# Optimization experiments

Hardware: AMD Instinct MI355X
Metric: run time of the kernel (lower is better)

Reference implementation:

```python
import jax, jax.numpy as jnp
import numpy as np

N_AGENTS = 64
_adj = np.ones((N_AGENTS, N_AGENTS)) - np.eye(N_AGENTS)
SEND_NP, RECV_NP = np.where(_adj)  # 4032 directed edges, no self-loops
N_EDGES = SEND_NP.shape[0]

D_NODE = 16
H = 64
D_OUT = 16
N_TYPES = 2
BATCH = 128


def _glorot(key, shape):
    fan_in, fan_out = shape[0], shape[1]
    lim = np.sqrt(6.0 / (fan_in + fan_out)).astype(np.float32)
    return jax.random.uniform(key, shape, jnp.float32, -lim, lim)


def setup_inputs() -> dict:
    key = jax.random.key(0)
    ks = jax.random.split(key, 16)
    inp = {
        "node_states": jax.random.normal(ks[0], (BATCH, N_AGENTS, 1, D_NODE), jnp.float32),
        "edge_types": jax.random.uniform(ks[1], (BATCH, N_EDGES, N_TYPES + 1, 1), jnp.float32),
        # edge encoder 0: MLP(32 -> 64 -> 64)
        "e0_w1": _glorot(ks[2], (2 * D_NODE, H)), "e0_b1": jnp.zeros((H,), jnp.float32),
        "e0_w2": _glorot(ks[3], (H, H)), "e0_b2": jnp.zeros((H,), jnp.float32),
        # edge encoder 1
        "e1_w1": _glorot(ks[4], (2 * D_NODE, H)), "e1_b1": jnp.zeros((H,), jnp.float32),
        "e1_w2": _glorot(ks[5], (H, H)), "e1_b2": jnp.zeros((H,), jnp.float32),
        # node decoder: MLP(16+64 -> 64 -> 16)
        "nd_w1": _glorot(ks[6], (D_NODE + H, H)), "nd_b1": jnp.zeros((H,), jnp.float32),
        "nd_w2": _glorot(ks[7], (H, D_OUT)), "nd_b2": jnp.zeros((D_OUT,), jnp.float32),
    }
    return inp


def _mlp2(x, w1, b1, w2, b2):
    h = jax.nn.relu(x @ w1 + b1)
    return jax.nn.relu(h @ w2 + b2)


def reference(node_states, edge_types,
              e0_w1, e0_b1, e0_w2, e0_b2,
              e1_w1, e1_b1, e1_w2, e1_b2,
              nd_w1, nd_b1, nd_w2, nd_b2):
    send = jnp.asarray(SEND_NP)
    recv = jnp.asarray(RECV_NP)
    # NodeAggregator: gather sender/receiver states to edges -> [B, E, 1, 2D]
    edge_msg = jnp.concatenate([node_states[:, send], node_states[:, recv]], axis=-1)
    # per-edge-type MLP encode, concat along axis 2 -> [B, E, T, H]
    enc0 = _mlp2(edge_msg, e0_w1, e0_b1, e0_w2, e0_b2)
    enc1 = _mlp2(edge_msg, e1_w1, e1_b1, e1_w2, e1_b2)
    encoded = jnp.concatenate([enc0, enc1], axis=2)
    # masked sum over edge types (skip type-0 'no edge') -> [B, E, 1, H]
    edge_msg_sum = jnp.sum(encoded * edge_types[:, :, 1:, :], axis=2, keepdims=True)
    # EdgeAggregator: scatter-sum edge messages to receiver nodes -> [B, N, 1, H]
    node_msg = jax.ops.segment_sum(
        edge_msg_sum.swapaxes(0, 1), recv, num_segments=N_AGENTS).swapaxes(0, 1)
    # decode
    node_state = jnp.concatenate([node_states, node_msg], axis=-1)  # [B, N, 1, D+H]
    return _mlp2(node_state, nd_w1, nd_b1, nd_w2, nd_b2)
```

## Files before the change

kernel.cpp:

```cpp
#include <hip/hip_runtime.h>
#include <hip/hip_fp16.h>


typedef _Float16 hf;
typedef __attribute__((ext_vector_type(8))) _Float16 v8hf;
typedef __attribute__((ext_vector_type(4))) float fv4;

union ABh { v8hf v; __half2 h[4]; };

__global__ __launch_bounds__(256, 4) void fused_kernel(
    const float* __restrict__ ns, const float* __restrict__ et,
    const float* __restrict__ e0w1, const float* __restrict__ e0b1,
    const float* __restrict__ e0w2, const float* __restrict__ e0b2,
    const float* __restrict__ e1w1, const float* __restrict__ e1b1,
    const float* __restrict__ e1w2, const float* __restrict__ e1b2,
    const float* __restrict__ ndw1, const float* __restrict__ ndb1,
    const float* __restrict__ ndw2, const float* __restrict__ ndb2,
    float* __restrict__ out)
{
  __shared__ float NSl[64*16];
  __shared__ __align__(16) _Float16 PlH[2*64*72];
  __shared__ __align__(16) _Float16 QbH[2*8*64];
  __shared__ float ETl[2*8*64];
  __shared__ float MSG[8*64];

  int t = threadIdx.x;
  int b = blockIdx.x >> 3, rg = blockIdx.x & 7, r0 = rg*8;
  int w = t >> 6, lane = t & 63, quad = lane >> 4, col = lane & 15;

  const __half2 z2 = __float22half2_rn(make_float2(0.f, 0.f));
  const v8hf zero8 = {};

  ((float4*)NSl)[t] = ((const float4*)(ns + b*1024))[t];
  __syncthreads();

  {
    ABh a;
    if (quad < 2) {
      const float* xr = NSl + (w*16 + col)*16 + quad*8;
      float4 x0 = *(const float4*)xr;
      float4 x1 = *(const float4*)(xr + 4);
      a.h[0] = __float22half2_rn(make_float2(x0.x, x0.y));
      a.h[1] = __float22half2_rn(make_float2(x0.z, x0.w));
      a.h[2] = __float22half2_rn(make_float2(x1.x, x1.y));
      a.h[3] = __float22half2_rn(make_float2(x1.z, x1.w));
    } else {
      a.h[0] = a.h[1] = a.h[2] = a.h[3] = z2;
    }
#pragma unroll 1
    for (int enc = 0; enc < 2; ++enc) {
      const float* w1 = enc ? e1w1 : e0w1;
#pragma unroll
      for (int ht = 0; ht < 4; ++ht) {
        ABh bb;
        if (quad < 2) {
#pragma unroll
          for (int j = 0; j < 4; ++j) {
            float f0 = w1[(quad*8 + 2*j    )*64 + ht*16 + col];
            float f1 = w1[(quad*8 + 2*j + 1)*64 + ht*16 + col];
            bb.h[j] = __float22half2_rn(make_float2(f0, f1));
          }
        } else {
          bb.h[0] = bb.h[1] = bb.h[2] = bb.h[3] = z2;
        }
        fv4 acc = {0.f, 0.f, 0.f, 0.f};
        acc = __builtin_amdgcn_mfma_f32_16x16x32_f16(a.v, bb.v, acc, 0, 0, 0);
        hf* pd = PlH + enc*4608 + (w*16 + quad*4)*72 + ht*16 + col;
        pd[0*72] = (hf)acc[0];
        pd[1*72] = (hf)acc[1];
        pd[2*72] = (hf)acc[2];
        pd[3*72] = (hf)acc[3];
      }
    }
  }
#pragma unroll
  for (int i = 0; i < 4; ++i) {
    int idx = i*256 + t;
    int enc = idx >> 9, rem = idx & 511;
    int rl = rem >> 6, h = rem & 63;
    const float* w1 = enc ? e1w1 : e0w1;
    const float* b1 = enc ? e1b1 : e0b1;
    const float* x = NSl + (r0 + rl)*16;
    float acc = b1[h];
#pragma unroll
    for (int k = 0; k < 16; ++k) acc += w1[(16 + k)*64 + h] * x[k];
    QbH[idx] = (hf)acc;
  }
#pragma unroll
  for (int i = 0; i < 2; ++i) {
    int idx = i*256 + t;
    int s = idx >> 3, rl = idx & 7;
    int r = r0 + rl;
    float v0 = 0.f, v1 = 0.f;
    if (s != r) {
      int pos = r - (r > s ? 1 : 0);
      const float* base = et + (b*4032 + s*63 + pos)*3;
      v0 = base[1]; v1 = base[2];
    }
    ETl[rl*64 + s] = v0;
    ETl[512 + rl*64 + s] = v1;
  }
  __syncthreads();

  float msgacc[2][4] = {{0.f,0.f,0.f,0.f},{0.f,0.f,0.f,0.f}};

#pragma unroll 1
  for (int enc = 0; enc < 2; ++enc) {
    const float* w2 = enc ? e1w2 : e0w2;
    const float* b2 = enc ? e1b2 : e0b2;
    v8hf bfr[4][2];
    float b2v[4];
#pragma unroll
    for (int nt = 0; nt < 4; ++nt) {
#pragma unroll
      for (int kk = 0; kk < 2; ++kk) {
        const float* base = w2 + (kk*32 + quad*8)*64 + nt*16 + col;
        ABh bb;
        bb.h[0] = __float22half2_rn(make_float2(base[0*64], base[1*64]));
        bb.h[1] = __float22half2_rn(make_float2(base[2*64], base[3*64]));
        bb.h[2] = __float22half2_rn(make_float2(base[4*64], base[5*64]));
        bb.h[3] = __float22half2_rn(make_float2(base[6*64], base[7*64]));
        bfr[nt][kk] = bb.v;
      }
      b2v[nt] = b2[nt*16 + col];
    }
#pragma unroll 1
    for (int rli = 0; rli < 2; ++rli) {
      int rl = w*2 + rli;
      const hf* qrow = QbH + (enc*8 + rl)*64;
      v8hf q0 = *(const v8hf*)(qrow + quad*8);
      v8hf q1 = *(const v8hf*)(qrow + 32 + quad*8);
      const float* etrow = ETl + (enc*8 + rl)*64;
#pragma unroll 2
      for (int st = 0; st < 4; ++st) {
        const hf* prow = PlH + enc*4608 + (st*16 + col)*72 + quad*8;
        v8hf p0 = *(const v8hf*)prow;
        v8hf p1 = *(const v8hf*)(prow + 32);
        v8hf s0 = __builtin_elementwise_max(p0 + q0, zero8);
        v8hf s1 = __builtin_elementwise_max(p1 + q1, zero8);
        float4 etv = *(const float4*)(etrow + st*16 + quad*4);
#pragma unroll
        for (int nt = 0; nt < 4; ++nt) {
          fv4 acc = {b2v[nt], b2v[nt], b2v[nt], b2v[nt]};
          acc = __builtin_amdgcn_mfma_f32_16x16x32_f16(s0, bfr[nt][0], acc, 0, 0, 0);
          acc = __builtin_amdgcn_mfma_f32_16x16x32_f16(s1, bfr[nt][1], acc, 0, 0, 0);
          float m = msgacc[rli][nt];
          m += etv.x * fmaxf(acc[0], 0.f);
          m += etv.y * fmaxf(acc[1], 0.f);
          m += etv.z * fmaxf(acc[2], 0.f);
          m += etv.w * fmaxf(acc[3], 0.f);
          msgacc[rli][nt] = m;
        }
      }
    }
  }
#pragma unroll
  for (int rli = 0; rli < 2; ++rli) {
#pragma unroll
    for (int nt = 0; nt < 4; ++nt) {
      float v = msgacc[rli][nt];
      v += __shfl_xor(v, 16);
      v += __shfl_xor(v, 32);
      if (lane < 16) MSG[(w*2 + rli)*64 + nt*16 + lane] = v;
    }
  }
  __syncthreads();

  float* HD = (float*)PlH;
#pragma unroll
  for (int pass = 0; pass < 2; ++pass) {
    int idx = pass*256 + t;
    int rl = idx >> 6, j = idx & 63;
    float acc = ndb1[j];
    const float* x0 = NSl + (r0 + rl)*16;
#pragma unroll
    for (int i = 0; i < 16; ++i) acc += x0[i] * ndw1[i*64 + j];
    const float* mrow = MSG + rl*64;
#pragma unroll
    for (int i = 0; i < 64; ++i) acc += mrow[i] * ndw1[(16 + i)*64 + j];
    HD[idx] = fmaxf(acc, 0.f);
  }
  __syncthreads();
  if (t < 128) {
    int rl = t >> 4, o = t & 15;
    float acc = ndb2[o];
#pragma unroll
    for (int j = 0; j < 64; ++j) acc += HD[rl*64 + j] * ndw2[j*16 + o];
    out[(b*64 + r0 + rl)*16 + o] = fmaxf(acc, 0.f);
  }
}

extern "C" void kernel_launch(void* const* d_in, const int* in_sizes, int n_in,
                              void* d_out, int out_size, void* d_ws, size_t ws_size,
                              hipStream_t stream) {
  const float* ns   = (const float*)d_in[0];
  const float* et   = (const float*)d_in[1];
  const float* e0w1 = (const float*)d_in[2];
  const float* e0b1 = (const float*)d_in[3];
  const float* e0w2 = (const float*)d_in[4];
  const float* e0b2 = (const float*)d_in[5];
  const float* e1w1 = (const float*)d_in[6];
  const float* e1b1 = (const float*)d_in[7];
  const float* e1w2 = (const float*)d_in[8];
  const float* e1b2 = (const float*)d_in[9];
  const float* ndw1 = (const float*)d_in[10];
  const float* ndb1 = (const float*)d_in[11];
  const float* ndw2 = (const float*)d_in[12];
  const float* ndb2 = (const float*)d_in[13];

  fused_kernel<<<1024, 256, 0, stream>>>(ns, et,
                                         e0w1, e0b1, e0w2, e0b2,
                                         e1w1, e1b1, e1w2, e1b2,
                                         ndw1, ndb1, ndw2, ndb2,
                                         (float*)d_out);
}
```

Before: 110.8 us.

## Move receiver projection and node decoder onto MFMA, drop shared node staging

```diff
diff --git a/kernel.cpp b/kernel.cpp
--- a/kernel.cpp
+++ b/kernel.cpp
@@ -18,11 +18,12 @@
     const float* __restrict__ ndw2, const float* __restrict__ ndb2,
     float* __restrict__ out)
 {
-  __shared__ float NSl[64*16];
   __shared__ __align__(16) _Float16 PlH[2*64*72];
   __shared__ __align__(16) _Float16 QbH[2*8*64];
   __shared__ float ETl[2*8*64];
-  __shared__ float MSG[8*64];
+  __shared__ __align__(16) _Float16 XDH[24*104];
+  _Float16* XD  = XDH;
+  _Float16* HD2 = XDH + 8*104;
 
   int t = threadIdx.x;
   int b = blockIdx.x >> 3, rg = blockIdx.x & 7, r0 = rg*8;
@@ -31,13 +32,29 @@
   const __half2 z2 = __float22half2_rn(make_float2(0.f, 0.f));
   const v8hf zero8 = {};
 
-  ((float4*)NSl)[t] = ((const float4*)(ns + b*1024))[t];
-  __syncthreads();
+  float xnv = 0.f;
+  if (t < 128) xnv = ns[(b*64 + r0 + (t >> 4))*16 + (t & 15)];
+  float ev0[2], ev1[2];
+  int es[2], erl[2];
+#pragma unroll
+  for (int i = 0; i < 2; ++i) {
+    int idx = i*256 + t;
+    int s = idx >> 3, rl = idx & 7;
+    es[i] = s; erl[i] = rl;
+    int r = r0 + rl;
+    float v0 = 0.f, v1 = 0.f;
+    if (s != r) {
+      int pos = r - (r > s ? 1 : 0);
+      const float* base = et + (b*4032 + s*63 + pos)*3;
+      v0 = base[1]; v1 = base[2];
+    }
+    ev0[i] = v0; ev1[i] = v1;
+  }
 
   {
     ABh a;
     if (quad < 2) {
-      const float* xr = NSl + (w*16 + col)*16 + quad*8;
+      const float* xr = ns + (b*64 + w*16 + col)*16 + quad*8;
       float4 x0 = *(const float4*)xr;
       float4 x1 = *(const float4*)(xr + 4);
       a.h[0] = __float22half2_rn(make_float2(x0.x, x0.y));
@@ -47,17 +64,20 @@
     } else {
       a.h[0] = a.h[1] = a.h[2] = a.h[3] = z2;
     }
+    bool qwave = (w == (rg >> 1));
 #pragma unroll 1
     for (int enc = 0; enc < 2; ++enc) {
       const float* w1 = enc ? e1w1 : e0w1;
+      const float* b1 = enc ? e1b1 : e0b1;
 #pragma unroll
       for (int ht = 0; ht < 4; ++ht) {
+        int cc = ht*16 + col;
         ABh bb;
         if (quad < 2) {
 #pragma unroll
           for (int j = 0; j < 4; ++j) {
-            float f0 = w1[(quad*8 + 2*j    )*64 + ht*16 + col];
-            float f1 = w1[(quad*8 + 2*j + 1)*64 + ht*16 + col];
+            float f0 = w1[(quad*8 + 2*j    )*64 + cc];
+            float f1 = w1[(quad*8 + 2*j + 1)*64 + cc];
             bb.h[j] = __float22half2_rn(make_float2(f0, f1));
           }
         } else {
@@ -65,40 +85,49 @@
         }
         fv4 acc = {0.f, 0.f, 0.f, 0.f};
         acc = __builtin_amdgcn_mfma_f32_16x16x32_f16(a.v, bb.v, acc, 0, 0, 0);
-        hf* pd = PlH + enc*4608 + (w*16 + quad*4)*72 + ht*16 + col;
+        hf* pd = PlH + enc*4608 + (w*16 + quad*4)*72 + cc;
         pd[0*72] = (hf)acc[0];
         pd[1*72] = (hf)acc[1];
         pd[2*72] = (hf)acc[2];
         pd[3*72] = (hf)acc[3];
       }
-    }
-  }
-#pragma unroll
-  for (int i = 0; i < 4; ++i) {
-    int idx = i*256 + t;
-    int enc = idx >> 9, rem = idx & 511;
-    int rl = rem >> 6, h = rem & 63;
-    const float* w1 = enc ? e1w1 : e0w1;
-    const float* b1 = enc ? e1b1 : e0b1;
-    const float* x = NSl + (r0 + rl)*16;
-    float acc = b1[h];
-#pragma unroll
-    for (int k = 0; k < 16; ++k) acc += w1[(16 + k)*64 + h] * x[k];
-    QbH[idx] = (hf)acc;
+      if (qwave) {
+#pragma unroll
+        for (int ht = 0; ht < 4; ++ht) {
+          int cc = ht*16 + col;
+          ABh bb;
+          if (quad < 2) {
+#pragma unroll
+            for (int j = 0; j < 4; ++j) {
+              float f0 = w1[(16 + quad*8 + 2*j    )*64 + cc];
+              float f1 = w1[(16 + quad*8 + 2*j + 1)*64 + cc];
+              bb.h[j] = __float22half2_rn(make_float2(f0, f1));
+            }
+          } else {
+            bb.h[0] = bb.h[1] = bb.h[2] = bb.h[3] = z2;
+          }
+          fv4 acc = {0.f, 0.f, 0.f, 0.f};
+          acc = __builtin_amdgcn_mfma_f32_16x16x32_f16(a.v, bb.v, acc, 0, 0, 0);
+          float b1v = b1[cc];
+#pragma unroll
+          for (int rr = 0; rr < 4; ++rr) {
+            int local = quad*4 + rr;
+            if ((local >> 3) == (rg & 1))
+              QbH[enc*512 + (local & 7)*64 + cc] = (hf)(acc[rr] + b1v);
+          }
+        }
+      }
+    }
+  }
+  if (t < 128) {
+    int rl = t >> 4, k = t & 15;
+    XD[rl*104 + k] = (hf)xnv;
+    XD[rl*104 + 80 + k] = (hf)0.f;
   }
 #pragma unroll
   for (int i = 0; i < 2; ++i) {
-    int idx = i*256 + t;
-    int s = idx >> 3, rl = idx & 7;
-    int r = r0 + rl;
-    float v0 = 0.f, v1 = 0.f;
-    if (s != r) {
-      int pos = r - (r > s ? 1 : 0);
-      const float* base = et + (b*4032 + s*63 + pos)*3;
-      v0 = base[1]; v1 = base[2];
-    }
-    ETl[rl*64 + s] = v0;
-    ETl[512 + rl*64 + s] = v1;
+    ETl[erl[i]*64 + es[i]] = ev0[i];
+    ETl[512 + erl[i]*64 + es[i]] = ev1[i];
   }
   __syncthreads();
 
@@ -161,32 +190,64 @@
       float v = msgacc[rli][nt];
       v += __shfl_xor(v, 16);
       v += __shfl_xor(v, 32);
-      if (lane < 16) MSG[(w*2 + rli)*64 + nt*16 + lane] = v;
+      if (lane < 16) XD[(w*2 + rli)*104 + 16 + nt*16 + lane] = (hf)v;
     }
   }
   __syncthreads();
 
-  float* HD = (float*)PlH;
-#pragma unroll
-  for (int pass = 0; pass < 2; ++pass) {
-    int idx = pass*256 + t;
-    int rl = idx >> 6, j = idx & 63;
-    float acc = ndb1[j];
-    const float* x0 = NSl + (r0 + rl)*16;
-#pragma unroll
-    for (int i = 0; i < 16; ++i) acc += x0[i] * ndw1[i*64 + j];
-    const float* mrow = MSG + rl*64;
-#pragma unroll
-    for (int i = 0; i < 64; ++i) acc += mrow[i] * ndw1[(16 + i)*64 + j];
-    HD[idx] = fmaxf(acc, 0.f);
-  }
-  __syncthreads();
-  if (t < 128) {
-    int rl = t >> 4, o = t & 15;
-    float acc = ndb2[o];
-#pragma unroll
-    for (int j = 0; j < 64; ++j) acc += HD[rl*64 + j] * ndw2[j*16 + o];
-    out[(b*64 + r0 + rl)*16 + o] = fmaxf(acc, 0.f);
+  if (w == 0) {
+    ABh xa[3];
+    const hf* xrow = XD + col*104;
+#pragma unroll
+    for (int kk = 0; kk < 3; ++kk) xa[kk].v = *(const v8hf*)(xrow + kk*32 + quad*8);
+#pragma unroll
+    for (int ht = 0; ht < 4; ++ht) {
+      int cc = ht*16 + col;
+      float bias = ndb1[cc];
+      fv4 acc = {bias, bias, bias, bias};
+#pragma unroll
+      for (int kk = 0; kk < 3; ++kk) {
+        ABh bb;
+#pragma unroll
+        for (int j = 0; j < 4; ++j) {
+          int rA = kk*32 + quad*8 + 2*j;
+          int rB = rA + 1;
+          float f0 = ndw1[(rA < 80 ? rA : 79)*64 + cc] * (rA < 80 ? 1.f : 0.f);
+          float f1 = ndw1[(rB < 80 ? rB : 79)*64 + cc] * (rB < 80 ? 1.f : 0.f);
+          bb.h[j] = __float22half2_rn(make_float2(f0, f1));
+        }
+        acc = __builtin_amdgcn_mfma_f32_16x16x32_f16(xa[kk].v, bb.v, acc, 0, 0, 0);
+      }
+      if (quad < 2) {
+#pragma unroll
+        for (int rr = 0; rr < 4; ++rr)
+          HD2[(quad*4 + rr)*104 + cc] = (hf)fmaxf(acc[rr], 0.f);
+      }
+    }
+    const hf* hrow = HD2 + col*104;
+    v8hf ha0 = *(const v8hf*)(hrow + quad*8);
+    v8hf ha1 = *(const v8hf*)(hrow + 32 + quad*8);
+    ABh b20, b21;
+#pragma unroll
+    for (int j = 0; j < 4; ++j) {
+      float f0 = ndw2[(quad*8 + 2*j    )*16 + col];
+      float f1 = ndw2[(quad*8 + 2*j + 1)*16 + col];
+      b20.h[j] = __float22half2_rn(make_float2(f0, f1));
+      float g0 = ndw2[(32 + quad*8 + 2*j    )*16 + col];
+      float g1 = ndw2[(32 + quad*8 + 2*j + 1)*16 + col];
+      b21.h[j] = __float22half2_rn(make_float2(g0, g1));
+    }
+    float bias2 = ndb2[col];
+    fv4 acc2 = {bias2, bias2, bias2, bias2};
+    acc2 = __builtin_amdgcn_mfma_f32_16x16x32_f16(ha0, b20.v, acc2, 0, 0, 0);
+    acc2 = __builtin_amdgcn_mfma_f32_16x16x32_f16(ha1, b21.v, acc2, 0, 0, 0);
+    if (quad < 2) {
+#pragma unroll
+      for (int rr = 0; rr < 4; ++rr) {
+        int rl = quad*4 + rr;
+        out[(b*64 + r0 + rl)*16 + col] = fmaxf(acc2[rr], 0.f);
+      }
+    }
   }
 }
 
```

After: 109.1 us. About the same (-1.5%).
